# Performance work log

Hardware: AMD Instinct MI355X
Metric: run time of the kernel (lower is better)

## Reference

```python
import jax, jax.numpy as jnp
import numpy as np

NEG_SLOPE = 0.2
MASK_FILL = -9e10


def setup_inputs() -> dict:
    key = jax.random.key(0)
    ks = jax.random.split(key, 8)
    B, N, D = 8, 2048, 64
    return {
        "opes_mask_adj": jax.random.randint(ks[0], (B, N, N), 0, 2, dtype=jnp.int32),
        "opes_mask_job": jax.random.randint(ks[1], (B, N, N), 0, 2, dtype=jnp.int32),
        "batch_idxes": jnp.arange(B, dtype=jnp.int64),
        "feats": jax.random.normal(ks[2], (B, N, D), dtype=jnp.float32),
        "W_ope": jax.random.normal(ks[3], (D, D), dtype=jnp.float32) * (1.0 / np.sqrt(D)),
        "attn_src": jax.random.normal(ks[4], (D,), dtype=jnp.float32) * (1.0 / np.sqrt(D)),
        "attn_dst": jax.random.normal(ks[5], (D,), dtype=jnp.float32) * (1.0 / np.sqrt(D)),
        "lambda_params": jax.random.normal(ks[6], (D, 2), dtype=jnp.float32),
    }


def reference(opes_mask_adj, opes_mask_job, batch_idxes, feats, W_ope, attn_src, attn_dst, lambda_params):
    # h_ope: [B, N, D]  (Linear with weight [out,in]: x @ W^T)
    h_ope = jnp.einsum("bnd,od->bno", feats, W_ope)
    a_src = h_ope @ attn_src  # [B, N]
    a_dst = h_ope @ attn_dst  # [B, N]
    e = a_src[:, :, None] + a_dst[:, None, :]  # [B, N, N]
    e = jnp.where(e >= 0, e, NEG_SLOPE * e)  # leaky relu

    mask_adj = opes_mask_adj[batch_idxes] == 1
    alpha_adj = jax.nn.softmax(jnp.where(mask_adj, e, MASK_FILL), axis=-1)
    h_adj = jnp.einsum("bnm,bmd->bnd", alpha_adj, h_ope)

    mask_job = opes_mask_job[batch_idxes] == 1
    alpha_job = jax.nn.softmax(jnp.where(mask_job, e, MASK_FILL), axis=-1)
    h_job = jnp.einsum("bnm,bmd->bnd", alpha_job, h_ope)

    # in_dim == out_dim -> identity residual (res_fc is None)
    lambdas = jax.nn.softmax(lambda_params, axis=1)  # [D, 2]
    lambda_adj, lambda_job = lambdas[:, 0], lambdas[:, 1]
    return lambda_adj * h_adj + lambda_job * h_job + feats
```

## Files before the change

### kernel.cpp

```cpp
#include <hip/hip_runtime.h>
#include <hip/hip_bf16.h>

#define B_ 8
#define N_ 2048
#define D_ 64

typedef __attribute__((ext_vector_type(8))) short bf16x8;
typedef __attribute__((ext_vector_type(4))) float f32x4;

__device__ inline unsigned short f32_bf16_rne(float f) {
    unsigned u = __float_as_uint(f);
    u += 0x7fffu + ((u >> 16) & 1u);
    return (unsigned short)(u >> 16);
}

__global__ __launch_bounds__(256) void prep_kernel(
    const float* __restrict__ feats, const float* __restrict__ W,
    const float* __restrict__ attn_src, const float* __restrict__ attn_dst,
    unsigned short* __restrict__ hT, float* __restrict__ a_src,
    float* __restrict__ a_dst) {
    __shared__ float w_lds[64 * 65];
    __shared__ float f_lds[32 * 64];
    __shared__ unsigned short hT_lds[64 * 40];

    const int t = threadIdx.x;
    const int b = blockIdx.x >> 6;
    const int rowbase = (blockIdx.x & 63) * 32;

#pragma unroll
    for (int k = 0; k < 4; k++) {
        int lin = (k * 256 + t) * 4;
        float4 v = *(const float4*)(W + lin);
        int o = lin >> 6, d = lin & 63;
        float* p = &w_lds[o * 65 + d];
        p[0] = v.x; p[1] = v.y; p[2] = v.z; p[3] = v.w;
    }
#pragma unroll
    for (int k = 0; k < 2; k++) {
        int lin = (k * 256 + t) * 4;
        float4 v = *(const float4*)(feats + (size_t)(b * N_ + rowbase) * D_ + lin);
        float* p = &f_lds[lin];
        p[0] = v.x; p[1] = v.y; p[2] = v.z; p[3] = v.w;
    }
    __syncthreads();

    const int w = t >> 6;
    const int o = t & 63;
    float acc[8] = {0.f, 0.f, 0.f, 0.f, 0.f, 0.f, 0.f, 0.f};
#pragma unroll 8
    for (int d = 0; d < 64; d++) {
        float wv = w_lds[o * 65 + d];
#pragma unroll
        for (int rr = 0; rr < 8; rr++)
            acc[rr] = fmaf(f_lds[(w * 8 + rr) * 64 + d], wv, acc[rr]);
    }
    float as_ = attn_src[o], ad_ = attn_dst[o];
#pragma unroll
    for (int rr = 0; rr < 8; rr++) {
        int row = rowbase + w * 8 + rr;
        float s1 = acc[rr] * as_;
        float s2 = acc[rr] * ad_;
#pragma unroll
        for (int off = 32; off; off >>= 1) {
            s1 += __shfl_xor(s1, off);
            s2 += __shfl_xor(s2, off);
        }
        if (o == 0) {
            a_src[b * N_ + row] = s1;
            a_dst[b * N_ + row] = s2;
        }
        hT_lds[o * 40 + w * 8 + rr] = f32_bf16_rne(acc[rr]);
    }
    __syncthreads();
    const int d = t >> 2, seg = t & 3;
    uint4 vv = *(const uint4*)(&hT_lds[d * 40 + seg * 8]);
    *(uint4*)(hT + ((size_t)(b * 64 + d) * N_ + rowbase + seg * 8)) = vv;
}

__global__ __launch_bounds__(256) void attn_kernel(
    const int* __restrict__ mask_adj, const int* __restrict__ mask_job,
    const int* __restrict__ batch_idxes,
    const unsigned short* __restrict__ hT, const float* __restrict__ a_src,
    const float* __restrict__ a_dst, float* __restrict__ pacc,
    float* __restrict__ zpart) {
    const int t = threadIdx.x;
    const int tile = blockIdx.x;
    const int b2 = tile >> 5;
    const int ib2 = (tile & 31) * 64;
    const int S = gridDim.y;
    const int jcount = (N_ / 128) / S;
    const int j0base = blockIdx.y * jcount * 128;

    const int wid = t >> 6, lane = t & 63;
    const int m = lane & 15, q = lane >> 4;
    const int irow0 = ib2 + wid * 16;
    const int i_a = irow0 + m;

    int bi = batch_idxes[b2];
    bi = (bi < 0) ? 0 : ((bi >= B_) ? (B_ - 1) : bi);
    const int* mA = mask_adj + (size_t)bi * N_ * N_ + (size_t)i_a * N_;
    const int* mJ = mask_job + (size_t)bi * N_ * N_ + (size_t)i_a * N_;
    const float asrc = a_src[b2 * N_ + i_a];
    const float* adst = a_dst + b2 * N_;
    const unsigned short* hTb = hT + (size_t)(b2 * 64) * N_;

    f32x4 accA[4], accJ[4];
#pragma unroll
    for (int dd = 0; dd < 4; dd++) {
        accA[dd] = (f32x4){0.f, 0.f, 0.f, 0.f};
        accJ[dd] = (f32x4){0.f, 0.f, 0.f, 0.f};
    }
    float zA = 0.f, zJ = 0.f;

    for (int jt = 0; jt < jcount; jt++) {
        const int j0 = j0base + jt * 128;
#pragma unroll
        for (int kk = 0; kk < 4; kk++) {
            const int jl = j0 + kk * 32 + q * 8;
            int4 a0 = *(const int4*)(mA + jl);
            int4 a1 = *(const int4*)(mA + jl + 4);
            int4 b0 = *(const int4*)(mJ + jl);
            int4 b1 = *(const int4*)(mJ + jl + 4);
            float4 d0 = *(const float4*)(adst + jl);
            float4 d1 = *(const float4*)(adst + jl + 4);
            bf16x8 fb0 = *(const bf16x8*)(hTb + (size_t)(0 * 16 + m) * N_ + jl);
            bf16x8 fb1 = *(const bf16x8*)(hTb + (size_t)(1 * 16 + m) * N_ + jl);
            bf16x8 fb2 = *(const bf16x8*)(hTb + (size_t)(2 * 16 + m) * N_ + jl);
            bf16x8 fb3 = *(const bf16x8*)(hTb + (size_t)(3 * 16 + m) * N_ + jl);
            int ma[8] = {a0.x, a0.y, a0.z, a0.w, a1.x, a1.y, a1.z, a1.w};
            int mj[8] = {b0.x, b0.y, b0.z, b0.w, b1.x, b1.y, b1.z, b1.w};
            float dv[8] = {d0.x, d0.y, d0.z, d0.w, d1.x, d1.y, d1.z, d1.w};
            bf16x8 fa, fj;
#pragma unroll
            for (int u = 0; u < 8; u++) {
                float e = asrc + dv[u];
                float le = fmaxf(e, 0.f) + 0.2f * fminf(e, 0.f);
                float p = __expf(le);
                float pa = (ma[u] == 1) ? p : 0.f;
                float pj = (mj[u] == 1) ? p : 0.f;
                zA += pa;
                zJ += pj;
                fa[u] = (short)f32_bf16_rne(pa);
                fj[u] = (short)f32_bf16_rne(pj);
            }
            accA[0] = __builtin_amdgcn_mfma_f32_16x16x32_bf16(fa, fb0, accA[0], 0, 0, 0);
            accJ[0] = __builtin_amdgcn_mfma_f32_16x16x32_bf16(fj, fb0, accJ[0], 0, 0, 0);
            accA[1] = __builtin_amdgcn_mfma_f32_16x16x32_bf16(fa, fb1, accA[1], 0, 0, 0);
            accJ[1] = __builtin_amdgcn_mfma_f32_16x16x32_bf16(fj, fb1, accJ[1], 0, 0, 0);
            accA[2] = __builtin_amdgcn_mfma_f32_16x16x32_bf16(fa, fb2, accA[2], 0, 0, 0);
            accJ[2] = __builtin_amdgcn_mfma_f32_16x16x32_bf16(fj, fb2, accJ[2], 0, 0, 0);
            accA[3] = __builtin_amdgcn_mfma_f32_16x16x32_bf16(fa, fb3, accA[3], 0, 0, 0);
            accJ[3] = __builtin_amdgcn_mfma_f32_16x16x32_bf16(fj, fb3, accJ[3], 0, 0, 0);
        }
    }

    zA += __shfl_xor(zA, 16); zA += __shfl_xor(zA, 32);
    zJ += __shfl_xor(zJ, 16); zJ += __shfl_xor(zJ, 32);

    const size_t blk = (size_t)tile * S + blockIdx.y;
    float* pb = pacc + blk * 8192;
    float* zr = zpart + blk * 128;
    if (q == 0) {
        zr[wid * 16 + m] = zA;
        zr[64 + wid * 16 + m] = zJ;
    }
#pragma unroll
    for (int dd = 0; dd < 4; dd++) {
        int d = dd * 16 + m;
#pragma unroll
        for (int r = 0; r < 4; r++) {
            int i = wid * 16 + q * 4 + r;
            pb[i * 64 + d] = accA[dd][r];
            pb[4096 + i * 64 + d] = accJ[dd][r];
        }
    }
}

__global__ __launch_bounds__(256) void combine_kernel(
    const float* __restrict__ pacc, const float* __restrict__ zpart,
    const float* __restrict__ feats, const float* __restrict__ lambda_params,
    float* __restrict__ out, int S) {
    const int tile = blockIdx.x;
    const int b = tile >> 5;
    const int rbase = (tile & 31) * 64;
    const int t = threadIdx.x;
    const int i = t >> 2;
    const int ds = (t & 3) * 16;

    const float* base = pacc + (size_t)tile * S * 8192;
    const float* zb = zpart + (size_t)tile * S * 128;

    float zA = 0.f, zJ = 0.f;
    float sA[16], sJ[16];
#pragma unroll
    for (int k = 0; k < 16; k++) { sA[k] = 0.f; sJ[k] = 0.f; }

    for (int s = 0; s < S; s++) {
        zA += zb[s * 128 + i];
        zJ += zb[s * 128 + 64 + i];
        const float* pA = base + (size_t)s * 8192 + i * 64 + ds;
        const float* pJ = pA + 4096;
#pragma unroll
        for (int k4 = 0; k4 < 4; k4++) {
            float4 vA = *(const float4*)(pA + k4 * 4);
            float4 vJ = *(const float4*)(pJ + k4 * 4);
            sA[k4 * 4 + 0] += vA.x; sA[k4 * 4 + 1] += vA.y;
            sA[k4 * 4 + 2] += vA.z; sA[k4 * 4 + 3] += vA.w;
            sJ[k4 * 4 + 0] += vJ.x; sJ[k4 * 4 + 1] += vJ.y;
            sJ[k4 * 4 + 2] += vJ.z; sJ[k4 * 4 + 3] += vJ.w;
        }
    }
    const float invA = 1.f / zA, invJ = 1.f / zJ;
    const size_t off = ((size_t)(b * N_ + rbase + i)) * D_ + ds;
#pragma unroll
    for (int k4 = 0; k4 < 4; k4++) {
        float4 f = *(const float4*)(feats + off + k4 * 4);
        float4 o;
        float* fo = (float*)&f;
        float* oo = (float*)&o;
#pragma unroll
        for (int c = 0; c < 4; c++) {
            int d = ds + k4 * 4 + c;
            float e0 = __expf(lambda_params[d * 2]);
            float e1 = __expf(lambda_params[d * 2 + 1]);
            float inv = 1.f / (e0 + e1);
            oo[c] = e0 * inv * sA[k4 * 4 + c] * invA +
                    e1 * inv * sJ[k4 * 4 + c] * invJ + fo[c];
        }
        *(float4*)(out + off + k4 * 4) = o;
    }
}

extern "C" void kernel_launch(void* const* d_in, const int* in_sizes, int n_in,
                              void* d_out, int out_size, void* d_ws, size_t ws_size,
                              hipStream_t stream) {
    const int* mask_adj = (const int*)d_in[0];
    const int* mask_job = (const int*)d_in[1];
    const int* batch_idxes = (const int*)d_in[2];
    const float* feats = (const float*)d_in[3];
    const float* W = (const float*)d_in[4];
    const float* attn_src = (const float*)d_in[5];
    const float* attn_dst = (const float*)d_in[6];
    const float* lambda_params = (const float*)d_in[7];
    float* out = (float*)d_out;

    unsigned short* hT = (unsigned short*)d_ws;
    char* p = (char*)d_ws + (size_t)B_ * 64 * N_ * 2;
    float* a_src = (float*)p;
    float* a_dst = a_src + B_ * N_;
    char* pz = p + 2 * (size_t)B_ * N_ * 4;

    auto need = [&](int S) {
        return (size_t)(pz - (char*)d_ws) +
               (size_t)256 * S * 128 * 4 +
               (size_t)256 * S * 8192 * 4;
    };
    int S = 4;
    if (ws_size < need(4)) S = 2;
    if (ws_size < need(2)) S = 1;

    float* zpart = (float*)pz;
    float* pacc = zpart + (size_t)256 * S * 128;

    prep_kernel<<<B_ * (N_ / 32), 256, 0, stream>>>(feats, W, attn_src, attn_dst,
                                                    hT, a_src, a_dst);
    dim3 grid(256, S, 1);
    attn_kernel<<<grid, 256, 0, stream>>>(mask_adj, mask_job, batch_idxes,
                                          hT, a_src, a_dst, pacc, zpart);
    combine_kernel<<<256, 256, 0, stream>>>(pacc, zpart, feats, lambda_params,
                                            out, S);
}
```

Measured before the change: 373.8 us.

## Pre-pack int32 masks into bitmasks with a ballot kernel before attention

Adds a pack kernel that streams both int32 mask tensors once and compresses each into 64-bit ballot bitmasks. The attention kernel then reads the packed bits instead of four int4 mask loads per step and tests bits to select probabilities. This removes the wide mask loads from the compute-heavy attention loop. In exchange it adds a separate launch that still reads the full masks, extra workspace, and a serialization point.

```diff
diff --git a/kernel.cpp b/kernel.cpp
--- a/kernel.cpp
+++ b/kernel.cpp
@@ -77,8 +77,44 @@
     *(uint4*)(hT + ((size_t)(b * 64 + d) * N_ + rowbase + seg * 8)) = vv;
 }
 
+__global__ __launch_bounds__(256) void pack_kernel(
+    const int* __restrict__ mask_adj, const int* __restrict__ mask_job,
+    unsigned long long* __restrict__ pkA, unsigned long long* __restrict__ pkJ) {
+    const int t = threadIdx.x;
+    const int wid = t >> 6, lane = t & 63;
+    const int r = blockIdx.x * 4 + wid;
+    const int* ra = mask_adj + (size_t)r * N_;
+    const int* rj = mask_job + (size_t)r * N_;
+    unsigned long long* wa = pkA + (size_t)r * (N_ / 64);
+    unsigned long long* wj = pkJ + (size_t)r * (N_ / 64);
+
+#pragma unroll
+    for (int sg = 0; sg < 8; sg++) {
+        const int j = sg * 256 + lane;
+        int a0 = ra[j];       int a1 = ra[j + 64];
+        int a2 = ra[j + 128]; int a3 = ra[j + 192];
+        int b0 = rj[j];       int b1 = rj[j + 64];
+        int b2 = rj[j + 128]; int b3 = rj[j + 192];
+        unsigned long long A0 = __ballot(a0 == 1);
+        unsigned long long A1 = __ballot(a1 == 1);
+        unsigned long long A2 = __ballot(a2 == 1);
+        unsigned long long A3 = __ballot(a3 == 1);
+        unsigned long long B0 = __ballot(b0 == 1);
+        unsigned long long B1 = __ballot(b1 == 1);
+        unsigned long long B2 = __ballot(b2 == 1);
+        unsigned long long B3 = __ballot(b3 == 1);
+        if (lane == 0) {
+            *(ulonglong2*)(wa + sg * 4)     = make_ulonglong2(A0, A1);
+            *(ulonglong2*)(wa + sg * 4 + 2) = make_ulonglong2(A2, A3);
+            *(ulonglong2*)(wj + sg * 4)     = make_ulonglong2(B0, B1);
+            *(ulonglong2*)(wj + sg * 4 + 2) = make_ulonglong2(B2, B3);
+        }
+    }
+}
+
 __global__ __launch_bounds__(256) void attn_kernel(
-    const int* __restrict__ mask_adj, const int* __restrict__ mask_job,
+    const unsigned long long* __restrict__ pkA,
+    const unsigned long long* __restrict__ pkJ,
     const int* __restrict__ batch_idxes,
     const unsigned short* __restrict__ hT, const float* __restrict__ a_src,
     const float* __restrict__ a_dst, float* __restrict__ pacc,
@@ -98,8 +134,8 @@
 
     int bi = batch_idxes[b2];
     bi = (bi < 0) ? 0 : ((bi >= B_) ? (B_ - 1) : bi);
-    const int* mA = mask_adj + (size_t)bi * N_ * N_ + (size_t)i_a * N_;
-    const int* mJ = mask_job + (size_t)bi * N_ * N_ + (size_t)i_a * N_;
+    const unsigned long long* pA = pkA + (size_t)(bi * N_ + i_a) * (N_ / 64);
+    const unsigned long long* pJ = pkJ + (size_t)(bi * N_ + i_a) * (N_ / 64);
     const float asrc = a_src[b2 * N_ + i_a];
     const float* adst = a_dst + b2 * N_;
     const unsigned short* hTb = hT + (size_t)(b2 * 64) * N_;
@@ -112,23 +148,25 @@
     }
     float zA = 0.f, zJ = 0.f;
 
+    const int shift = q << 3;
+
     for (int jt = 0; jt < jcount; jt++) {
         const int j0 = j0base + jt * 128;
+        ulonglong2 wA = *(const ulonglong2*)(pA + (j0 >> 6));
+        ulonglong2 wJ = *(const ulonglong2*)(pJ + (j0 >> 6));
 #pragma unroll
         for (int kk = 0; kk < 4; kk++) {
             const int jl = j0 + kk * 32 + q * 8;
-            int4 a0 = *(const int4*)(mA + jl);
-            int4 a1 = *(const int4*)(mA + jl + 4);
-            int4 b0 = *(const int4*)(mJ + jl);
-            int4 b1 = *(const int4*)(mJ + jl + 4);
+            unsigned long long a64 = (kk & 2) ? wA.y : wA.x;
+            unsigned long long j64 = (kk & 2) ? wJ.y : wJ.x;
+            unsigned bA8 = (unsigned)(a64 >> (((kk & 1) << 5) + shift)) & 0xffu;
+            unsigned bJ8 = (unsigned)(j64 >> (((kk & 1) << 5) + shift)) & 0xffu;
             float4 d0 = *(const float4*)(adst + jl);
             float4 d1 = *(const float4*)(adst + jl + 4);
             bf16x8 fb0 = *(const bf16x8*)(hTb + (size_t)(0 * 16 + m) * N_ + jl);
             bf16x8 fb1 = *(const bf16x8*)(hTb + (size_t)(1 * 16 + m) * N_ + jl);
             bf16x8 fb2 = *(const bf16x8*)(hTb + (size_t)(2 * 16 + m) * N_ + jl);
             bf16x8 fb3 = *(const bf16x8*)(hTb + (size_t)(3 * 16 + m) * N_ + jl);
-            int ma[8] = {a0.x, a0.y, a0.z, a0.w, a1.x, a1.y, a1.z, a1.w};
-            int mj[8] = {b0.x, b0.y, b0.z, b0.w, b1.x, b1.y, b1.z, b1.w};
             float dv[8] = {d0.x, d0.y, d0.z, d0.w, d1.x, d1.y, d1.z, d1.w};
             bf16x8 fa, fj;
 #pragma unroll
@@ -136,8 +174,8 @@
                 float e = asrc + dv[u];
                 float le = fmaxf(e, 0.f) + 0.2f * fminf(e, 0.f);
                 float p = __expf(le);
-                float pa = (ma[u] == 1) ? p : 0.f;
-                float pj = (mj[u] == 1) ? p : 0.f;
+                float pa = (bA8 & (1u << u)) ? p : 0.f;
+                float pj = (bJ8 & (1u << u)) ? p : 0.f;
                 zA += pa;
                 zJ += pj;
                 fa[u] = (short)f32_bf16_rne(pa);
@@ -248,7 +286,10 @@
     char* p = (char*)d_ws + (size_t)B_ * 64 * N_ * 2;
     float* a_src = (float*)p;
     float* a_dst = a_src + B_ * N_;
-    char* pz = p + 2 * (size_t)B_ * N_ * 4;
+    char* ppk = p + 2 * (size_t)B_ * N_ * 4;
+    unsigned long long* pkA = (unsigned long long*)ppk;
+    unsigned long long* pkJ = pkA + (size_t)B_ * N_ * (N_ / 64);
+    char* pz = ppk + 2 * (size_t)B_ * N_ * (N_ / 64) * 8;
 
     auto need = [&](int S) {
         return (size_t)(pz - (char*)d_ws) +
@@ -262,10 +303,11 @@
     float* zpart = (float*)pz;
     float* pacc = zpart + (size_t)256 * S * 128;
 
+    pack_kernel<<<B_ * N_ / 4, 256, 0, stream>>>(mask_adj, mask_job, pkA, pkJ);
     prep_kernel<<<B_ * (N_ / 32), 256, 0, stream>>>(feats, W, attn_src, attn_dst,
                                                     hT, a_src, a_dst);
     dim3 grid(256, S, 1);
-    attn_kernel<<<grid, 256, 0, stream>>>(mask_adj, mask_job, batch_idxes,
+    attn_kernel<<<grid, 256, 0, stream>>>(pkA, pkJ, batch_idxes,
                                           hT, a_src, a_dst, pacc, zpart);
     combine_kernel<<<256, 256, 0, stream>>>(pacc, zpart, feats, lambda_params,
                                             out, S);
```

After: 359.4 us. 1.04x faster.
